# Kernel tuning notes

Hardware: AMD Instinct MI355X
Metric: run time of the kernel (lower is better)

Reference implementation:

```python
import jax, jax.numpy as jnp
import numpy as np
from jax import lax

CONF_THRES = 0.25
IOU_THRES = 0.45
MAX_WH = 4096.0   # class offset, agnostic=False
MAX_DET = 300
NEG = jnp.float32(-1e30)


def setup_inputs() -> dict:
    key = jax.random.key(0)
    B, N, C = 16, 25200, 85  # 640x640 yolov5, nc=80
    k1, k2, k3, k4 = jax.random.split(key, 4)
    xy = jax.random.uniform(k1, (B, N, 2), jnp.float32, 0.0, 640.0)
    wh = jax.random.uniform(k2, (B, N, 2), jnp.float32, 4.0, 120.0)
    obj = jax.random.uniform(k3, (B, N, 1), jnp.float32)
    cls = jax.random.uniform(k4, (B, N, C - 5), jnp.float32)
    prediction = jnp.concatenate([xy, wh, obj, cls], axis=-1)
    return {"prediction": prediction}


def _xywh2xyxy(b):
    # b: [N,4] (cx,cy,w,h) -> (x1,y1,x2,y2)
    return jnp.concatenate([b[:, :2] - b[:, 2:4] * 0.5,
                            b[:, :2] + b[:, 2:4] * 0.5], axis=1)


def _iou_one_vs_all(box, boxes):
    # box: [4], boxes: [N,4], plain IoU as in torchvision.ops.nms
    x1 = jnp.maximum(box[0], boxes[:, 0])
    y1 = jnp.maximum(box[1], boxes[:, 1])
    x2 = jnp.minimum(box[2], boxes[:, 2])
    y2 = jnp.minimum(box[3], boxes[:, 3])
    inter = jnp.clip(x2 - x1, 0.0) * jnp.clip(y2 - y1, 0.0)
    a1 = (box[2] - box[0]) * (box[3] - box[1])
    a2 = (boxes[:, 2] - boxes[:, 0]) * (boxes[:, 3] - boxes[:, 1])
    return inter / (a1 + a2 - inter)


def _nms_image(p):
    # p: [N, 5+nc] single-image predictions (decoded xywh, obj, class scores)
    obj = p[:, 4]                               # [N]
    cls_scores = p[:, 5:] * obj[:, None]        # x[:,5:] *= x[:,4:5]
    conf = jnp.max(cls_scores, axis=1)          # best-class conf
    j = jnp.argmax(cls_scores, axis=1)          # best class id
    boxes = _xywh2xyxy(p[:, :4])                # [N,4]
    valid = (obj > CONF_THRES) & (conf > CONF_THRES)
    # class-offset boxes for per-class NMS (agnostic=False)
    nms_boxes = boxes + (j.astype(boxes.dtype) * MAX_WH)[:, None]

    s0 = jnp.where(valid, conf, NEG)

    def step(s_live, _):
        i = jnp.argmax(s_live)
        sel = s_live[i]
        keep = sel > 0.0
        iou = _iou_one_vs_all(nms_boxes[i], nms_boxes)
        suppress = keep & (iou > IOU_THRES)
        s_new = jnp.where(suppress, NEG, s_live).at[i].set(NEG)
        return s_new, (i, keep)

    _, (idxs, keeps) = lax.scan(step, s0, None, length=MAX_DET)
    # output rows [x1,y1,x2,y2,conf,cls] — boxes WITHOUT class offset
    rows = jnp.concatenate([boxes[idxs], conf[idxs, None],
                            j[idxs, None].astype(boxes.dtype)], axis=1)
    rows = rows * keeps[:, None].astype(rows.dtype)  # zero padded slots
    return rows, keeps


def reference(prediction):
    # prediction: [B, N, 5+nc] -> ([B, MAX_DET, 6], [B, MAX_DET] keep mask)
    out, keep = jax.vmap(_nms_image)(prediction)
    return out, keep
```

## Files before the change

kernel.cpp:

```cpp
#include <hip/hip_runtime.h>
#include <cstdint>
#include <cfloat>

#define BATCH 16
#define NBOX 25200
#define CH 85
#define NCLS 80
#define CAP 512
#define SEGCAP 128
#define ACC 48
#define MAXDET 300
#define RPB 112
#define CNTPAD 16

typedef unsigned long long u64;

__device__ __forceinline__ u64 shflx64(u64 v, int m) {
    int lo = __shfl_xor((int)(unsigned)(v & 0xffffffffu), m);
    int hi = __shfl_xor((int)(unsigned)(v >> 32), m);
    return ((u64)(unsigned)hi << 32) | (u64)(unsigned)lo;
}

__global__ __launch_bounds__(256) void pre_kernel(const float* __restrict__ p,
                                                  int* __restrict__ cnt,
                                                  u64* __restrict__ bucketKey,
                                                  float* __restrict__ outZero,
                                                  int outN) {
#pragma clang fp contract(off)
    __shared__ float s[RPB * CH];
    int tid = threadIdx.x;

    long z = (long)blockIdx.x * 256 + tid;
    if (z < outN) outZero[z] = 0.0f;

    long blockRow = (long)blockIdx.x * RPB;

    const float4* p4 = (const float4*)(p + blockRow * CH);
    float4* s4 = (float4*)s;
    for (int t = tid; t < RPB * CH / 4; t += 256) {
        __builtin_amdgcn_global_load_lds(
            (const __attribute__((address_space(1))) void*)(p4 + t),
            (__attribute__((address_space(3))) void*)(s4 + (t & ~63)),
            16, 0, 0);
    }
    __syncthreads();

    int r = tid >> 1;
    int half = tid & 1;
    if (r < RPB) {
        const float* row = s + r * CH;
        float obj = row[4];

        float v = -FLT_MAX; int c = 1000;
        int c0 = half * 40;
        for (int k = 0; k < 40; k++) {
            float sc = row[5 + c0 + k] * obj;
            int cc = c0 + k;
            if (sc > v) { v = sc; c = cc; }
        }
        float v2 = __shfl_xor(v, 1);
        int   cz = __shfl_xor(c, 1);
        if (v2 > v || (v2 == v && cz < c)) { v = v2; c = cz; }

        if (half == 0 && obj > 0.25f && v > 0.25f) {
            int wid = (int)blockRow + r;
            int b   = wid / NBOX;
            int idx = wid - b * NBOX;
            u64 key = ((u64)__float_as_uint(v) << 22) | ((u64)(32767 - idx) << 7) | (u64)c;
            int bkt = b * NCLS + c;
            int seg = idx & 3;
            int pos = atomicAdd(&cnt[bkt * CNTPAD + seg], 1);
            if (pos < SEGCAP) bucketKey[(long)bkt * CAP + seg * SEGCAP + pos] = key;
        }
    }
}

__global__ __launch_bounds__(256) void nms_kernel(const float* __restrict__ p,
                                                  const int* __restrict__ cnt,
                                                  const u64* __restrict__ bucketKey,
                                                  u64* __restrict__ accKey) {
#pragma clang fp contract(off)
    int lane = threadIdx.x & 63;
    int bkt = (blockIdx.x << 2) | (threadIdx.x >> 6);
    int b = bkt / NCLS, c = bkt - b * NCLS;

    const int* cb = cnt + bkt * CNTPAD;
    int ns[4];
#pragma unroll
    for (int s2 = 0; s2 < 4; s2++) {
        int v = cb[s2];
        ns[s2] = (v < SEGCAP) ? v : SEGCAP;
    }
    int ntot = ns[0] + ns[1] + ns[2] + ns[3];

    u64 key[8];
#pragma unroll
    for (int r = 0; r < 8; r++) {
        int off = ((r & 1) << 6) | lane;
        key[r] = (off < ns[r >> 1]) ? bucketKey[(long)bkt * CAP + (r << 6) + lane] : 0ULL;
    }

    auto CE_lane = [&](int k, int j) {
#pragma unroll
        for (int r = 0; r < 8; r++) {
            u64 part = shflx64(key[r], j);
            int pos = (r << 6) | lane;
            bool keepmax = (((pos & k) == 0) == ((lane & j) == 0));
            u64 mx = (key[r] > part) ? key[r] : part;
            u64 mn = (key[r] > part) ? part : key[r];
            key[r] = keepmax ? mx : mn;
        }
    };

#pragma unroll
    for (int k = 2; k <= 64; k <<= 1)
        for (int j = k >> 1; j > 0; j >>= 1)
            CE_lane(k, j);

#define CE_REG(K, M)                                                   \
    {                                                                  \
        _Pragma("unroll")                                              \
        for (int r = 0; r < 8; r++) if (!(r & (M))) {                  \
            int r2 = r | (M);                                          \
            u64 a = key[r], d = key[r2];                               \
            bool desc = (((r << 6) & (K)) == 0);                       \
            u64 hi = (a > d) ? a : d, lo = (a > d) ? d : a;            \
            key[r]  = desc ? hi : lo;                                  \
            key[r2] = desc ? lo : hi;                                  \
        }                                                              \
    }

    CE_REG(128, 1)
    for (int j = 32; j > 0; j >>= 1) CE_lane(128, j);
    CE_REG(256, 2) CE_REG(256, 1)
    for (int j = 32; j > 0; j >>= 1) CE_lane(256, j);
    CE_REG(512, 4) CE_REG(512, 2) CE_REG(512, 1)
    for (int j = 32; j > 0; j >>= 1) CE_lane(512, j);
#undef CE_REG

    float off = (float)c * 4096.0f;
    float rx1[8], ry1[8], rx2[8], ry2[8], rar[8];
    int live = 0;
#pragma unroll
    for (int r = 0; r < 8; r++) {
        int pos = (r << 6) | lane;
        rx1[r] = 0.f; ry1[r] = 0.f; rx2[r] = 0.f; ry2[r] = 0.f; rar[r] = 0.f;
        if (pos < ntot) {
            int idx = 32767 - (int)((key[r] >> 7) & 32767);
            const float* q = p + ((long)b * NBOX + idx) * CH;
            float x = q[0], y = q[1], w = q[2], h = q[3];
            float hw = w * 0.5f, hh = h * 0.5f;
            rx1[r] = (x - hw) + off; ry1[r] = (y - hh) + off;
            rx2[r] = (x + hw) + off; ry2[r] = (y + hh) + off;
            rar[r] = (rx2[r] - rx1[r]) * (ry2[r] - ry1[r]);
            live |= 1 << r;
        }
    }

    long obase = (long)bkt * ACC;
    int nacc = 0;
    for (;;) {
        int i = -1;
#pragma unroll
        for (int r = 0; r < 8; r++) {
            if (i < 0) {
                u64 mr = __ballot((live >> r) & 1);
                if (mr) i = (r << 6) + (int)__ffsll((long long)mr) - 1;
            }
        }
        if (i < 0) break;
        int ro = i >> 6, owner = i & 63;

        u64 kk; float sX1, sY1, sX2, sY2, sA;
        switch (ro) {
            case 0: kk=key[0]; sX1=rx1[0]; sY1=ry1[0]; sX2=rx2[0]; sY2=ry2[0]; sA=rar[0]; break;
            case 1: kk=key[1]; sX1=rx1[1]; sY1=ry1[1]; sX2=rx2[1]; sY2=ry2[1]; sA=rar[1]; break;
            case 2: kk=key[2]; sX1=rx1[2]; sY1=ry1[2]; sX2=rx2[2]; sY2=ry2[2]; sA=rar[2]; break;
            case 3: kk=key[3]; sX1=rx1[3]; sY1=ry1[3]; sX2=rx2[3]; sY2=ry2[3]; sA=rar[3]; break;
            case 4: kk=key[4]; sX1=rx1[4]; sY1=ry1[4]; sX2=rx2[4]; sY2=ry2[4]; sA=rar[4]; break;
            case 5: kk=key[5]; sX1=rx1[5]; sY1=ry1[5]; sX2=rx2[5]; sY2=ry2[5]; sA=rar[5]; break;
            case 6: kk=key[6]; sX1=rx1[6]; sY1=ry1[6]; sX2=rx2[6]; sY2=ry2[6]; sA=rar[6]; break;
            default:kk=key[7]; sX1=rx1[7]; sY1=ry1[7]; sX2=rx2[7]; sY2=ry2[7]; sA=rar[7]; break;
        }
        if (lane == owner) {
            accKey[obase + nacc] = kk;
            live &= ~(1 << ro);
        }
        nacc++;
        if (nacc == ACC) break;

        float X1 = __int_as_float(__builtin_amdgcn_readlane(__float_as_int(sX1), owner));
        float Y1 = __int_as_float(__builtin_amdgcn_readlane(__float_as_int(sY1), owner));
        float X2 = __int_as_float(__builtin_amdgcn_readlane(__float_as_int(sX2), owner));
        float Y2 = __int_as_float(__builtin_amdgcn_readlane(__float_as_int(sY2), owner));
        float A  = __int_as_float(__builtin_amdgcn_readlane(__float_as_int(sA),  owner));

#pragma unroll
        for (int r = 0; r < 8; r++) {
            if ((live >> r) & 1) {
                float xx1 = fmaxf(X1, rx1[r]);
                float yy1 = fmaxf(Y1, ry1[r]);
                float xx2 = fminf(X2, rx2[r]);
                float yy2 = fminf(Y2, ry2[r]);
                float inter = fmaxf(xx2 - xx1, 0.0f) * fmaxf(yy2 - yy1, 0.0f);
                float uni = (A + rar[r]) - inter;
                if (inter / uni > 0.45f) live &= ~(1 << r);
            }
        }
    }
    for (int t = nacc + lane; t < ACC; t += 64) accKey[obase + t] = 0ULL;
}

__global__ __launch_bounds__(256) void merge_kernel(const float* __restrict__ p,
                                                    const u64* __restrict__ accKey,
                                                    float* __restrict__ outRows,
                                                    float* __restrict__ outKeep) {
#pragma clang fp contract(off)
    __shared__ u64 L[NCLS * ACC];
    int tid = threadIdx.x;
    int b = blockIdx.y;
    const u64* src = accKey + (long)b * NCLS * ACC;
    for (int t = tid; t < NCLS * ACC; t += 256) L[t] = src[t];
    __syncthreads();

    int g = blockIdx.x * 256 + tid;
    u64 key = L[g];
    if (key == 0ULL) return;
    int cOwn = g / ACC;
    int rank = g - cOwn * ACC;

    int d = 1;
    for (; d + 3 < NCLS; d += 4) {
        int ca = cOwn + d;     if (ca >= NCLS) ca -= NCLS;
        int cb = cOwn + d + 1; if (cb >= NCLS) cb -= NCLS;
        int cc = cOwn + d + 2; if (cc >= NCLS) cc -= NCLS;
        int cd = cOwn + d + 3; if (cd >= NCLS) cd -= NCLS;
        const u64* LA = L + ca * ACC;
        const u64* LB = L + cb * ACC;
        const u64* LC = L + cc * ACC;
        const u64* LD = L + cd * ACC;
        int na = 0, nb = 0, nc = 0, nd = 0;
#pragma unroll
        for (int s2 = 32; s2; s2 >>= 1) {
            int ta = na + s2, tb = nb + s2, tc = nc + s2, td = nd + s2;
            if (ta <= ACC && LA[ta - 1] > key) na = ta;
            if (tb <= ACC && LB[tb - 1] > key) nb = tb;
            if (tc <= ACC && LC[tc - 1] > key) nc = tc;
            if (td <= ACC && LD[td - 1] > key) nd = td;
        }
        rank += na + nb + nc + nd;
        if (rank >= MAXDET) return;
    }
    for (; d < NCLS; d++) {
        int c2 = cOwn + d; if (c2 >= NCLS) c2 -= NCLS;
        const u64* Lc = L + c2 * ACC;
        int cn = 0;
#pragma unroll
        for (int s2 = 32; s2; s2 >>= 1) {
            int ncx = cn + s2;
            if (ncx <= ACC && Lc[ncx - 1] > key) cn = ncx;
        }
        rank += cn;
        if (rank >= MAXDET) return;
    }

    int cc  = (int)(key & 127);
    int idx = 32767 - (int)((key >> 7) & 32767);
    float conf = __uint_as_float((unsigned)(key >> 22));
    const float* q = p + ((long)b * NBOX + idx) * CH;
    float x = q[0], y = q[1], w = q[2], h = q[3];
    float hw = w * 0.5f, hh = h * 0.5f;
    float* row = outRows + ((long)b * MAXDET + rank) * 6;
    row[0] = x - hw; row[1] = y - hh; row[2] = x + hw; row[3] = y + hh;
    row[4] = conf;   row[5] = (float)cc;
    outKeep[b * MAXDET + rank] = 1.0f;
}

extern "C" void kernel_launch(void* const* d_in, const int* in_sizes, int n_in,
                              void* d_out, int out_size, void* d_ws, size_t ws_size,
                              hipStream_t stream) {
    const float* p = (const float*)d_in[0];
    float* out = (float*)d_out;

    char* ws = (char*)d_ws;
    int* cnt = (int*)ws;
    u64* bucketKey = (u64*)(ws + BATCH * NCLS * CNTPAD * 4);
    u64* accKey    = (u64*)(ws + BATCH * NCLS * CNTPAD * 4
                               + (size_t)BATCH * NCLS * CAP * 8);

    hipMemsetAsync(cnt, 0, BATCH * NCLS * CNTPAD * sizeof(int), stream);
    pre_kernel<<<(BATCH * NBOX) / RPB, 256, 0, stream>>>(p, cnt, bucketKey, out, out_size);
    nms_kernel<<<BATCH * NCLS / 4, 256, 0, stream>>>(p, cnt, bucketKey, accKey);
    dim3 gM(NCLS * ACC / 256, BATCH);
    merge_kernel<<<gM, 256, 0, stream>>>(p, accKey, out, out + (size_t)BATCH * MAXDET * 6);
}
```

Baseline: 288.4 us.

## Replace bitonic sort with per-iteration argmax and store boxes in bucket records

Each bucket record now holds the class-offset box coordinates alongside the sort key, written once in the pre-pass. The NMS kernel therefore no longer gathers coordinates from the prediction tensor with scattered reads. The full bitonic sort of up to 512 keys per bucket is removed; each greedy iteration instead finds the top live key with a register reduction followed by a wave-wide shuffle reduction. Launch shape changes to one 64-thread block per bucket. The trade-off is larger records (32 bytes each) and a per-iteration reduction of about six shuffle rounds over several values, in exchange for skipping the sort, which costs far more when buckets are small.

Result: slower. 321.8 us (+11.6%).

```diff
diff --git a/kernel.cpp b/kernel.cpp
--- a/kernel.cpp
+++ b/kernel.cpp
@@ -23,7 +23,7 @@
 
 __global__ __launch_bounds__(256) void pre_kernel(const float* __restrict__ p,
                                                   int* __restrict__ cnt,
-                                                  u64* __restrict__ bucketKey,
+                                                  u64* __restrict__ rec,
                                                   float* __restrict__ outZero,
                                                   int outN) {
 #pragma clang fp contract(off)
@@ -70,19 +70,27 @@
             int bkt = b * NCLS + c;
             int seg = idx & 3;
             int pos = atomicAdd(&cnt[bkt * CNTPAD + seg], 1);
-            if (pos < SEGCAP) bucketKey[(long)bkt * CAP + seg * SEGCAP + pos] = key;
-        }
-    }
-}
-
-__global__ __launch_bounds__(256) void nms_kernel(const float* __restrict__ p,
-                                                  const int* __restrict__ cnt,
-                                                  const u64* __restrict__ bucketKey,
-                                                  u64* __restrict__ accKey) {
+            if (pos < SEGCAP) {
+                float x = row[0], y = row[1], w = row[2], h = row[3];
+                float hw = w * 0.5f, hh = h * 0.5f;
+                float offc = (float)c * 4096.0f;
+                float4 b4;
+                b4.x = (x - hw) + offc; b4.y = (y - hh) + offc;
+                b4.z = (x + hw) + offc; b4.w = (y + hh) + offc;
+                u64* slot = rec + ((long)bkt * CAP + seg * SEGCAP + pos) * 4;
+                *(float4*)slot = b4;
+                slot[2] = key;
+            }
+        }
+    }
+}
+
+__global__ __launch_bounds__(64) void nms_kernel(const int* __restrict__ cnt,
+                                                 const u64* __restrict__ rec,
+                                                 u64* __restrict__ accKey) {
 #pragma clang fp contract(off)
-    int lane = threadIdx.x & 63;
-    int bkt = (blockIdx.x << 2) | (threadIdx.x >> 6);
-    int b = bkt / NCLS, c = bkt - b * NCLS;
+    int lane = threadIdx.x;
+    int bkt = blockIdx.x;
 
     const int* cb = cnt + bkt * CNTPAD;
     int ns[4];
@@ -91,120 +99,63 @@
         int v = cb[s2];
         ns[s2] = (v < SEGCAP) ? v : SEGCAP;
     }
-    int ntot = ns[0] + ns[1] + ns[2] + ns[3];
-
+
+    const u64* R = rec + (long)bkt * CAP * 4;
     u64 key[8];
-#pragma unroll
-    for (int r = 0; r < 8; r++) {
-        int off = ((r & 1) << 6) | lane;
-        key[r] = (off < ns[r >> 1]) ? bucketKey[(long)bkt * CAP + (r << 6) + lane] : 0ULL;
-    }
-
-    auto CE_lane = [&](int k, int j) {
-#pragma unroll
-        for (int r = 0; r < 8; r++) {
-            u64 part = shflx64(key[r], j);
-            int pos = (r << 6) | lane;
-            bool keepmax = (((pos & k) == 0) == ((lane & j) == 0));
-            u64 mx = (key[r] > part) ? key[r] : part;
-            u64 mn = (key[r] > part) ? part : key[r];
-            key[r] = keepmax ? mx : mn;
-        }
-    };
-
-#pragma unroll
-    for (int k = 2; k <= 64; k <<= 1)
-        for (int j = k >> 1; j > 0; j >>= 1)
-            CE_lane(k, j);
-
-#define CE_REG(K, M)                                                   \
-    {                                                                  \
-        _Pragma("unroll")                                              \
-        for (int r = 0; r < 8; r++) if (!(r & (M))) {                  \
-            int r2 = r | (M);                                          \
-            u64 a = key[r], d = key[r2];                               \
-            bool desc = (((r << 6) & (K)) == 0);                       \
-            u64 hi = (a > d) ? a : d, lo = (a > d) ? d : a;            \
-            key[r]  = desc ? hi : lo;                                  \
-            key[r2] = desc ? lo : hi;                                  \
-        }                                                              \
-    }
-
-    CE_REG(128, 1)
-    for (int j = 32; j > 0; j >>= 1) CE_lane(128, j);
-    CE_REG(256, 2) CE_REG(256, 1)
-    for (int j = 32; j > 0; j >>= 1) CE_lane(256, j);
-    CE_REG(512, 4) CE_REG(512, 2) CE_REG(512, 1)
-    for (int j = 32; j > 0; j >>= 1) CE_lane(512, j);
-#undef CE_REG
-
-    float off = (float)c * 4096.0f;
-    float rx1[8], ry1[8], rx2[8], ry2[8], rar[8];
-    int live = 0;
+    float x1[8], y1[8], x2[8], y2[8], ar[8];
 #pragma unroll
     for (int r = 0; r < 8; r++) {
         int pos = (r << 6) | lane;
-        rx1[r] = 0.f; ry1[r] = 0.f; rx2[r] = 0.f; ry2[r] = 0.f; rar[r] = 0.f;
-        if (pos < ntot) {
-            int idx = 32767 - (int)((key[r] >> 7) & 32767);
-            const float* q = p + ((long)b * NBOX + idx) * CH;
-            float x = q[0], y = q[1], w = q[2], h = q[3];
-            float hw = w * 0.5f, hh = h * 0.5f;
-            rx1[r] = (x - hw) + off; ry1[r] = (y - hh) + off;
-            rx2[r] = (x + hw) + off; ry2[r] = (y + hh) + off;
-            rar[r] = (rx2[r] - rx1[r]) * (ry2[r] - ry1[r]);
-            live |= 1 << r;
-        }
+        int off = ((r & 1) << 6) | lane;
+        float4 b4 = *(const float4*)(R + (long)pos * 4);
+        u64 k = R[(long)pos * 4 + 2];
+        key[r] = (off < ns[r >> 1]) ? k : 0ULL;
+        x1[r] = b4.x; y1[r] = b4.y; x2[r] = b4.z; y2[r] = b4.w;
+        ar[r] = (x2[r] - x1[r]) * (y2[r] - y1[r]);
     }
 
     long obase = (long)bkt * ACC;
     int nacc = 0;
-    for (;;) {
-        int i = -1;
+    for (int it = 0; it < ACC; ++it) {
+        u64 m = key[0];
+        float X1 = x1[0], Y1 = y1[0], X2 = x2[0], Y2 = y2[0];
+#pragma unroll
+        for (int r = 1; r < 8; r++) {
+            bool g = key[r] > m;
+            m  = g ? key[r] : m;
+            X1 = g ? x1[r] : X1; Y1 = g ? y1[r] : Y1;
+            X2 = g ? x2[r] : X2; Y2 = g ? y2[r] : Y2;
+        }
+#pragma unroll
+        for (int j = 1; j < 64; j <<= 1) {
+            u64 ok = shflx64(m, j);
+            float oX1 = __shfl_xor(X1, j), oY1 = __shfl_xor(Y1, j);
+            float oX2 = __shfl_xor(X2, j), oY2 = __shfl_xor(Y2, j);
+            bool g = ok > m;
+            m  = g ? ok : m;
+            X1 = g ? oX1 : X1; Y1 = g ? oY1 : Y1;
+            X2 = g ? oX2 : X2; Y2 = g ? oY2 : Y2;
+        }
+        if (m == 0ULL) break;
+
+        float A = (X2 - X1) * (Y2 - Y1);
+
 #pragma unroll
         for (int r = 0; r < 8; r++) {
-            if (i < 0) {
-                u64 mr = __ballot((live >> r) & 1);
-                if (mr) i = (r << 6) + (int)__ffsll((long long)mr) - 1;
-            }
-        }
-        if (i < 0) break;
-        int ro = i >> 6, owner = i & 63;
-
-        u64 kk; float sX1, sY1, sX2, sY2, sA;
-        switch (ro) {
-            case 0: kk=key[0]; sX1=rx1[0]; sY1=ry1[0]; sX2=rx2[0]; sY2=ry2[0]; sA=rar[0]; break;
-            case 1: kk=key[1]; sX1=rx1[1]; sY1=ry1[1]; sX2=rx2[1]; sY2=ry2[1]; sA=rar[1]; break;
-            case 2: kk=key[2]; sX1=rx1[2]; sY1=ry1[2]; sX2=rx2[2]; sY2=ry2[2]; sA=rar[2]; break;
-            case 3: kk=key[3]; sX1=rx1[3]; sY1=ry1[3]; sX2=rx2[3]; sY2=ry2[3]; sA=rar[3]; break;
-            case 4: kk=key[4]; sX1=rx1[4]; sY1=ry1[4]; sX2=rx2[4]; sY2=ry2[4]; sA=rar[4]; break;
-            case 5: kk=key[5]; sX1=rx1[5]; sY1=ry1[5]; sX2=rx2[5]; sY2=ry2[5]; sA=rar[5]; break;
-            case 6: kk=key[6]; sX1=rx1[6]; sY1=ry1[6]; sX2=rx2[6]; sY2=ry2[6]; sA=rar[6]; break;
-            default:kk=key[7]; sX1=rx1[7]; sY1=ry1[7]; sX2=rx2[7]; sY2=ry2[7]; sA=rar[7]; break;
-        }
-        if (lane == owner) {
-            accKey[obase + nacc] = kk;
-            live &= ~(1 << ro);
+            if (key[r] == m) { accKey[obase + nacc] = m; key[r] = 0ULL; }
         }
         nacc++;
-        if (nacc == ACC) break;
-
-        float X1 = __int_as_float(__builtin_amdgcn_readlane(__float_as_int(sX1), owner));
-        float Y1 = __int_as_float(__builtin_amdgcn_readlane(__float_as_int(sY1), owner));
-        float X2 = __int_as_float(__builtin_amdgcn_readlane(__float_as_int(sX2), owner));
-        float Y2 = __int_as_float(__builtin_amdgcn_readlane(__float_as_int(sY2), owner));
-        float A  = __int_as_float(__builtin_amdgcn_readlane(__float_as_int(sA),  owner));
 
 #pragma unroll
         for (int r = 0; r < 8; r++) {
-            if ((live >> r) & 1) {
-                float xx1 = fmaxf(X1, rx1[r]);
-                float yy1 = fmaxf(Y1, ry1[r]);
-                float xx2 = fminf(X2, rx2[r]);
-                float yy2 = fminf(Y2, ry2[r]);
+            if (key[r] != 0ULL) {
+                float xx1 = fmaxf(X1, x1[r]);
+                float yy1 = fmaxf(Y1, y1[r]);
+                float xx2 = fminf(X2, x2[r]);
+                float yy2 = fminf(Y2, y2[r]);
                 float inter = fmaxf(xx2 - xx1, 0.0f) * fmaxf(yy2 - yy1, 0.0f);
-                float uni = (A + rar[r]) - inter;
-                if (inter / uni > 0.45f) live &= ~(1 << r);
+                float uni = (A + ar[r]) - inter;
+                if (inter / uni > 0.45f) key[r] = 0ULL;
             }
         }
     }
@@ -284,13 +235,13 @@
 
     char* ws = (char*)d_ws;
     int* cnt = (int*)ws;
-    u64* bucketKey = (u64*)(ws + BATCH * NCLS * CNTPAD * 4);
-    u64* accKey    = (u64*)(ws + BATCH * NCLS * CNTPAD * 4
-                               + (size_t)BATCH * NCLS * CAP * 8);
+    u64* rec = (u64*)(ws + BATCH * NCLS * CNTPAD * 4);
+    u64* accKey = (u64*)(ws + BATCH * NCLS * CNTPAD * 4
+                            + (size_t)BATCH * NCLS * CAP * 32);
 
     hipMemsetAsync(cnt, 0, BATCH * NCLS * CNTPAD * sizeof(int), stream);
-    pre_kernel<<<(BATCH * NBOX) / RPB, 256, 0, stream>>>(p, cnt, bucketKey, out, out_size);
-    nms_kernel<<<BATCH * NCLS / 4, 256, 0, stream>>>(p, cnt, bucketKey, accKey);
+    pre_kernel<<<(BATCH * NBOX) / RPB, 256, 0, stream>>>(p, cnt, rec, out, out_size);
+    nms_kernel<<<BATCH * NCLS, 64, 0, stream>>>(cnt, rec, accKey);
     dim3 gM(NCLS * ACC / 256, BATCH);
     merge_kernel<<<gM, 256, 0, stream>>>(p, accKey, out, out + (size_t)BATCH * MAXDET * 6);
 }
```
